# Kernel tuning notes

Hardware: AMD Instinct MI355X
Metric: run time of the kernel (lower is better)

The kernel has to match this reference:

```python
import jax, jax.numpy as jnp
import numpy as np

B, N, D, H = 4, 2048, 1024, 64

def setup_inputs() -> dict:
    key = jax.random.key(0)
    ks = jax.random.split(key, 7)
    s = D ** -0.5  # torch Linear default init scale ~ U(-1/sqrt(fan_in), ...); scale randn similarly
    return {
        "x":  jax.random.normal(ks[0], (B, N, D), dtype=jnp.float32),
        "Wq": jax.random.normal(ks[1], (D, H), dtype=jnp.float32) * s,
        "bq": jax.random.normal(ks[2], (H,), dtype=jnp.float32) * s,
        "Wk": jax.random.normal(ks[3], (D, H), dtype=jnp.float32) * s,
        "bk": jax.random.normal(ks[4], (H,), dtype=jnp.float32) * s,
        "Wv": jax.random.normal(ks[5], (D, H), dtype=jnp.float32) * s,
        "bv": jax.random.normal(ks[6], (H,), dtype=jnp.float32) * s,
    }

def reference(x, Wq, bq, Wk, bk, Wv, bv):
    head_size = Wq.shape[1]
    q = x @ Wq + bq          # [B, N, H]
    k = x @ Wk + bk          # [B, N, H]
    v = x @ Wv + bv          # [B, N, H]
    scores = jnp.einsum("bid,bjd->bij", q, k)        # [B, N, N]
    # faithful to torch: keep upper triangle (col >= row), then mask exact zeros to -inf
    scores = jnp.triu(scores)
    scores = jnp.where(scores == 0, -jnp.inf, scores)
    attn = jax.nn.softmax(scores * (head_size ** -0.5), axis=-1)  # [B, N, N]
    # out = (V^T @ attn)^T  ==  attn^T @ V
    out = jnp.einsum("bji,bjh->bih", attn, v)         # [B, N, H]
    return out
```

## Files before the change

kernel.cpp:

```cpp
#include <hip/hip_runtime.h>
#include <math.h>

constexpr int kN = 2048;
constexpr int kD = 1024;

typedef __attribute__((ext_vector_type(8))) short bf16x8;
typedef __attribute__((ext_vector_type(4))) short bf16x4;
typedef __attribute__((ext_vector_type(4))) float f32x4;

#define MFMA(a, b, c) __builtin_amdgcn_mfma_f32_16x16x32_bf16(a, b, c, 0, 0, 0)

__device__ __forceinline__ short f2bf(float f) {
    unsigned u = __float_as_uint(f);
    u += 0x7fff + ((u >> 16) & 1);
    return (short)(u >> 16);
}

__device__ __forceinline__ void g2l(void* lds, const void* g, int nbytes, int t) {
    int lane = t & 63, w = t >> 6;
    for (int base = w * 1024; base < nbytes; base += 4096) {
        if (base + lane * 16 < nbytes) {
            __builtin_amdgcn_global_load_lds(
                (const __attribute__((address_space(1))) void*)((const char*)g + base + lane * 16),
                (__attribute__((address_space(3))) void*)((char*)lds + base),
                16, 0, 0);
        }
    }
}

__global__ __launch_bounds__(256) void prep_kernel(
        const float* __restrict__ x,
        const float* __restrict__ Wq, const float* __restrict__ Wk,
        const float* __restrict__ Wv, const float* __restrict__ bq,
        const float* __restrict__ bk, const float* __restrict__ bv,
        short* __restrict__ xb, short* __restrict__ Wt, float* __restrict__ bcat)
{
    int tid = blockIdx.x * 256 + threadIdx.x;
    int stride = gridDim.x * 256;
    for (int e = tid; e < 16 * 8192 * 64; e += stride) {
        int kc = e >> 19;
        int rem = e & 524287;
        int row = rem >> 6, c = rem & 63;
        xb[((size_t)(kc * 8192 + row)) * 72 + c] = f2bf(x[(size_t)row * kD + kc * 64 + c]);
    }
    for (int e = tid; e < 16 * 64 * 192; e += stride) {
        int n = e % 192;
        int rc = e / 192;
        int c = rc & 63, kc = rc >> 6;
        int d = kc * 64 + c;
        float wv = (n < 64) ? Wq[d * 64 + n]
                 : (n < 128) ? Wk[d * 64 + (n - 64)]
                 : Wv[d * 64 + (n - 128)];
        Wt[(kc * 192 + n) * 72 + c] = f2bf(wv);
    }
    if (tid < 192)
        bcat[tid] = (tid < 64) ? bq[tid] : (tid < 128) ? bk[tid - 64] : bv[tid - 128];
}

__global__ __launch_bounds__(256) void qkv_kernel(
        const short* __restrict__ xb, const short* __restrict__ Wt,
        const float* __restrict__ bcat,
        short* __restrict__ gq, short* __restrict__ gk, short* __restrict__ vt)
{
    __shared__ __align__(16) short xs[32 * 72];
    __shared__ __align__(16) short wsm[192 * 72];
    const int t = threadIdx.x;
    const int w = t >> 6, lane = t & 63, l15 = lane & 15, q8 = lane >> 4;
    const int m0 = blockIdx.x * 32;

    f32x4 acc[2][3];
    #pragma unroll
    for (int rt = 0; rt < 2; ++rt)
        #pragma unroll
        for (int ct = 0; ct < 3; ++ct) acc[rt][ct] = (f32x4){0.f, 0.f, 0.f, 0.f};

    for (int kc = 0; kc < 16; ++kc) {
        __syncthreads();
        g2l(xs, xb + ((size_t)(kc * 8192 + m0)) * 72, 32 * 144, t);
        g2l(wsm, Wt + (size_t)kc * 192 * 72, 192 * 144, t);
        __syncthreads();

        bf16x8 a[2][2], b[3][2];
        #pragma unroll
        for (int rt = 0; rt < 2; ++rt) {
            int arow = rt * 16 + l15;
            a[rt][0] = *(const bf16x8*)&xs[arow * 72 + q8 * 8];
            a[rt][1] = *(const bf16x8*)&xs[arow * 72 + 32 + q8 * 8];
        }
        #pragma unroll
        for (int ct = 0; ct < 3; ++ct) {
            int brow = w * 48 + ct * 16 + l15;
            b[ct][0] = *(const bf16x8*)&wsm[brow * 72 + q8 * 8];
            b[ct][1] = *(const bf16x8*)&wsm[brow * 72 + 32 + q8 * 8];
        }
        #pragma unroll
        for (int rt = 0; rt < 2; ++rt)
            #pragma unroll
            for (int ct = 0; ct < 3; ++ct) {
                acc[rt][ct] = MFMA(a[rt][0], b[ct][0], acc[rt][ct]);
                acc[rt][ct] = MFMA(a[rt][1], b[ct][1], acc[rt][ct]);
            }
    }

    const int bz = m0 >> 11;
    const int jt = (m0 & 2047) >> 6;
    const int jb = m0 & 63;
    #pragma unroll
    for (int rt = 0; rt < 2; ++rt)
        #pragma unroll
        for (int ct = 0; ct < 3; ++ct) {
            int nb = w * 48 + ct * 16;
            int n = nb + l15;
            float bias = bcat[n];
            if (nb < 64) {
                #pragma unroll
                for (int r = 0; r < 4; ++r)
                    gq[(size_t)(m0 + rt * 16 + q8 * 4 + r) * 72 + n] =
                        f2bf(acc[rt][ct][r] + bias);
            } else if (nb < 128) {
                #pragma unroll
                for (int r = 0; r < 4; ++r)
                    gk[(size_t)(m0 + rt * 16 + q8 * 4 + r) * 72 + (n - 64)] =
                        f2bf(acc[rt][ct][r] + bias);
            } else {
                int h = n - 128;
                bf16x4 pk = {f2bf(acc[rt][ct][0] + bias), f2bf(acc[rt][ct][1] + bias),
                             f2bf(acc[rt][ct][2] + bias), f2bf(acc[rt][ct][3] + bias)};
                *(bf16x4*)&vt[((size_t)((bz * 32 + jt) * 64 + h)) * 72 + jb + rt * 16 + q8 * 4] = pk;
            }
        }
}

__global__ __launch_bounds__(256) void stats_kernel(
        const short* __restrict__ gq, const short* __restrict__ gk,
        float* __restrict__ l2)
{
    __shared__ __align__(16) short qsm[64 * 72];
    __shared__ __align__(16) short ksm[64 * 72];
    const int t = threadIdx.x;
    const int w = t >> 6, lane = t & 63, l15 = lane & 15, q8 = lane >> 4;
    const int b = blockIdx.x;
    const int ic = b & 3, bz = (b >> 2) & 3, jt = b >> 4;
    const int j0 = jt * 64;
    const int ilo = ic * 512, ihi = ilo + 512;
    const int istart = (j0 > ilo) ? j0 : ilo;

    float lloc[4] = {0.f, 0.f, 0.f, 0.f};

    if (istart < ihi) {
        g2l(qsm, gq + (size_t)(bz * kN + j0) * 72, 64 * 144, t);
        __syncthreads();
        int jrow = 16 * w + l15;
        bf16x8 a0 = *(const bf16x8*)&qsm[jrow * 72 + q8 * 8];
        bf16x8 a1 = *(const bf16x8*)&qsm[jrow * 72 + 32 + q8 * 8];

        for (int i0 = istart; i0 < ihi; i0 += 64) {
            __syncthreads();
            g2l(ksm, gk + (size_t)(bz * kN + i0) * 72, 64 * 144, t);
            __syncthreads();
            #pragma unroll
            for (int it = 0; it < 4; ++it) {
                int irow = it * 16 + l15;
                bf16x8 b0 = *(const bf16x8*)&ksm[irow * 72 + q8 * 8];
                bf16x8 b1 = *(const bf16x8*)&ksm[irow * 72 + 32 + q8 * 8];
                f32x4 s = (f32x4){0.f, 0.f, 0.f, 0.f};
                s = MFMA(a0, b0, s);
                s = MFMA(a1, b1, s);
                int ig = i0 + it * 16 + l15;
                #pragma unroll
                for (int r = 0; r < 4; ++r) {
                    int jg = j0 + 16 * w + q8 * 4 + r;
                    float sv = s[r];
                    float e = __expf(sv * 0.125f);
                    lloc[r] += ((ig >= jg) && (sv != 0.0f)) ? e : 0.0f;
                }
            }
        }
    }
    #pragma unroll
    for (int off = 1; off < 16; off <<= 1)
        #pragma unroll
        for (int r = 0; r < 4; ++r)
            lloc[r] += __shfl_xor(lloc[r], off);
    if (l15 == 0) {
        #pragma unroll
        for (int r = 0; r < 4; ++r)
            l2[ic * 8192 + bz * kN + j0 + 16 * w + q8 * 4 + r] = lloc[r];
    }
}

__global__ __launch_bounds__(256) void combine_kernel(
        const float* __restrict__ l2, float* __restrict__ rlf)
{
    int r = blockIdx.x * 256 + threadIdx.x;
    float l = l2[r] + l2[8192 + r] + l2[16384 + r] + l2[24576 + r];
    rlf[r] = (l > 0.f) ? 1.0f / l : 0.0f;
}

__global__ __launch_bounds__(256) void out_kernel(
        const short* __restrict__ gq, const short* __restrict__ gk,
        const short* __restrict__ vt, const float* __restrict__ rlf,
        float* __restrict__ part)
{
    __shared__ __align__(16) short ksm[64 * 72];
    __shared__ __align__(16) short qsm[64 * 72];
    __shared__ __align__(16) short vsm[64 * 72];
    __shared__ __align__(16) short psm[64 * 72];
    __shared__ float rsm[64];
    const int t = threadIdx.x;
    const int w = t >> 6, lane = t & 63, l15 = lane & 15, q8 = lane >> 4;
    const int b = blockIdx.x;
    const int jc = b & 3, bz = (b >> 2) & 3, it = b >> 4;
    const int i0 = it * 64;
    const int jlo = jc * 512;
    const int jhi = (jlo + 512 < i0 + 64) ? (jlo + 512) : (i0 + 64);

    f32x4 oacc[4];
    #pragma unroll
    for (int i = 0; i < 4; ++i) oacc[i] = (f32x4){0.f, 0.f, 0.f, 0.f};

    if (jlo < jhi) {
        g2l(ksm, gk + (size_t)(bz * kN + i0) * 72, 64 * 144, t);
        for (int j0s = jlo; j0s < jhi; j0s += 64) {
            __syncthreads();
            g2l(qsm, gq + (size_t)(bz * kN + j0s) * 72, 64 * 144, t);
            g2l(vsm, vt + (size_t)((bz * 32 + (j0s >> 6)) * 64) * 72, 64 * 144, t);
            if (t < 64) rsm[t] = rlf[bz * kN + j0s + t];
            __syncthreads();

            int jrow = 16 * w + l15;
            bf16x8 a0 = *(const bf16x8*)&qsm[jrow * 72 + q8 * 8];
            bf16x8 a1 = *(const bf16x8*)&qsm[jrow * 72 + 32 + q8 * 8];
            #pragma unroll
            for (int itile = 0; itile < 4; ++itile) {
                int irow = itile * 16 + l15;
                bf16x8 b0 = *(const bf16x8*)&ksm[irow * 72 + q8 * 8];
                bf16x8 b1 = *(const bf16x8*)&ksm[irow * 72 + 32 + q8 * 8];
                f32x4 s = (f32x4){0.f, 0.f, 0.f, 0.f};
                s = MFMA(a0, b0, s);
                s = MFMA(a1, b1, s);
                int ig = i0 + itile * 16 + l15;
                bf16x4 pk;
                #pragma unroll
                for (int r = 0; r < 4; ++r) {
                    int jl = 16 * w + q8 * 4 + r;
                    int jg = j0s + jl;
                    float sv = s[r];
                    float p = ((ig >= jg) && (sv != 0.0f))
                            ? __expf(sv * 0.125f) * rsm[jl] : 0.0f;
                    pk[r] = f2bf(p);
                }
                *(bf16x4*)&psm[(itile * 16 + l15) * 72 + 16 * w + q8 * 4] = pk;
            }
            __syncthreads();

            bf16x8 pa0 = *(const bf16x8*)&psm[(16 * w + l15) * 72 + q8 * 8];
            bf16x8 pa1 = *(const bf16x8*)&psm[(16 * w + l15) * 72 + 32 + q8 * 8];
            #pragma unroll
            for (int ht = 0; ht < 4; ++ht) {
                int vrow = ht * 16 + l15;
                bf16x8 vb0 = *(const bf16x8*)&vsm[vrow * 72 + q8 * 8];
                bf16x8 vb1 = *(const bf16x8*)&vsm[vrow * 72 + 32 + q8 * 8];
                oacc[ht] = MFMA(pa0, vb0, oacc[ht]);
                oacc[ht] = MFMA(pa1, vb1, oacc[ht]);
            }
        }
    }
    size_t base = ((size_t)(jc * 4 + bz) * kN + i0) * 64;
    #pragma unroll
    for (int ht = 0; ht < 4; ++ht)
        #pragma unroll
        for (int r = 0; r < 4; ++r)
            part[base + (size_t)(16 * w + q8 * 4 + r) * 64 + ht * 16 + l15] = oacc[ht][r];
}

__global__ __launch_bounds__(256) void reduce_kernel(
        const float* __restrict__ part, float* __restrict__ out)
{
    int idx = blockIdx.x * 256 + threadIdx.x;
    const float4* p = (const float4*)part;
    float4 a = p[idx];
    float4 b = p[idx + 131072];
    float4 c = p[idx + 262144];
    float4 d = p[idx + 393216];
    float4 r;
    r.x = a.x + b.x + c.x + d.x;
    r.y = a.y + b.y + c.y + d.y;
    r.z = a.z + b.z + c.z + d.z;
    r.w = a.w + b.w + c.w + d.w;
    ((float4*)out)[idx] = r;
}

extern "C" void kernel_launch(void* const* d_in, const int* in_sizes, int n_in,
                              void* d_out, int out_size, void* d_ws, size_t ws_size,
                              hipStream_t stream)
{
    const float* x  = (const float*)d_in[0];
    const float* Wq = (const float*)d_in[1];
    const float* bq = (const float*)d_in[2];
    const float* Wk = (const float*)d_in[3];
    const float* bk = (const float*)d_in[4];
    const float* Wv = (const float*)d_in[5];
    const float* bv = (const float*)d_in[6];
    float* out = (float*)d_out;

    char* base = (char*)d_ws;
    short* Wt   = (short*)(base);
    float* bcat = (float*)(base + 442368);
    short* xb   = (short*)(base + 443392);
    short* gq   = (short*)(base + 19317760);
    short* gk   = (short*)(base + 20497408);
    short* vt   = (short*)(base + 21677056);
    float* l2   = (float*)(base + 22856704);
    float* rlf  = (float*)(base + 22987776);
    float* part = (float*)(base + 23020544);

    prep_kernel<<<2048, 256, 0, stream>>>(x, Wq, Wk, Wv, bq, bk, bv, xb, Wt, bcat);
    qkv_kernel<<<256, 256, 0, stream>>>(xb, Wt, bcat, gq, gk, vt);
    stats_kernel<<<512, 256, 0, stream>>>(gq, gk, l2);
    combine_kernel<<<32, 256, 0, stream>>>(l2, rlf);
    out_kernel<<<512, 256, 0, stream>>>(gq, gk, vt, rlf, part);
    reduce_kernel<<<512, 256, 0, stream>>>(part, out);
}
```

Measured before the change: 143.1 us.

## Fuse x conversion into QKV GEMM, double-buffer LDS loads, drop combine kernel

The separate pass that converted x to a padded bf16 copy is removed. The QKV kernel now loads fp32 x directly, converts it in registers and double-buffers both the x and weight tiles, with 16-row blocks giving twice as many blocks. The stats and out kernels double-buffer their K, Q and V tile loads so the next tile's global loads overlap the current MFMAs. The combine kernel is folded into out_kernel, which computes the reciprocal normalizer inline, saving one launch and a large intermediate write and read of x, at the cost of more LDS per block and redundant reciprocal work.

```diff
diff --git a/kernel.cpp b/kernel.cpp
--- a/kernel.cpp
+++ b/kernel.cpp
@@ -29,106 +29,104 @@
 }
 
 __global__ __launch_bounds__(256) void prep_kernel(
-        const float* __restrict__ x,
         const float* __restrict__ Wq, const float* __restrict__ Wk,
         const float* __restrict__ Wv, const float* __restrict__ bq,
         const float* __restrict__ bk, const float* __restrict__ bv,
-        short* __restrict__ xb, short* __restrict__ Wt, float* __restrict__ bcat)
+        short* __restrict__ Wt, float* __restrict__ bcat)
 {
     int tid = blockIdx.x * 256 + threadIdx.x;
     int stride = gridDim.x * 256;
-    for (int e = tid; e < 16 * 8192 * 64; e += stride) {
-        int kc = e >> 19;
-        int rem = e & 524287;
-        int row = rem >> 6, c = rem & 63;
-        xb[((size_t)(kc * 8192 + row)) * 72 + c] = f2bf(x[(size_t)row * kD + kc * 64 + c]);
-    }
-    for (int e = tid; e < 16 * 64 * 192; e += stride) {
-        int n = e % 192;
-        int rc = e / 192;
-        int c = rc & 63, kc = rc >> 6;
-        int d = kc * 64 + c;
-        float wv = (n < 64) ? Wq[d * 64 + n]
-                 : (n < 128) ? Wk[d * 64 + (n - 64)]
-                 : Wv[d * 64 + (n - 128)];
-        Wt[(kc * 192 + n) * 72 + c] = f2bf(wv);
+    for (int e = tid; e < 16 * 192 * 72; e += stride) {
+        int kc = e / (192 * 72);
+        int rem = e - kc * (192 * 72);
+        int n = rem / 72, c = rem - n * 72;
+        short v = 0;
+        if (c < 64) {
+            int d = kc * 64 + c;
+            float wv = (n < 64) ? Wq[d * 64 + n]
+                     : (n < 128) ? Wk[d * 64 + (n - 64)]
+                     : Wv[d * 64 + (n - 128)];
+            v = f2bf(wv);
+        }
+        Wt[e] = v;
     }
     if (tid < 192)
         bcat[tid] = (tid < 64) ? bq[tid] : (tid < 128) ? bk[tid - 64] : bv[tid - 128];
 }
 
 __global__ __launch_bounds__(256) void qkv_kernel(
-        const short* __restrict__ xb, const short* __restrict__ Wt,
+        const float* __restrict__ x, const short* __restrict__ Wt,
         const float* __restrict__ bcat,
         short* __restrict__ gq, short* __restrict__ gk, short* __restrict__ vt)
 {
-    __shared__ __align__(16) short xs[32 * 72];
-    __shared__ __align__(16) short wsm[192 * 72];
+    __shared__ __align__(16) short xs[2][16 * 72];
+    __shared__ __align__(16) short wsm[2][192 * 72];
     const int t = threadIdx.x;
     const int w = t >> 6, lane = t & 63, l15 = lane & 15, q8 = lane >> 4;
-    const int m0 = blockIdx.x * 32;
-
-    f32x4 acc[2][3];
-    #pragma unroll
-    for (int rt = 0; rt < 2; ++rt)
-        #pragma unroll
-        for (int ct = 0; ct < 3; ++ct) acc[rt][ct] = (f32x4){0.f, 0.f, 0.f, 0.f};
+    const int m0 = blockIdx.x * 16;
+    const int xrow = t >> 4, xc4 = t & 15;
+    const float* xbase = x + (size_t)(m0 + xrow) * kD + xc4 * 4;
+
+    f32x4 acc[3];
+    #pragma unroll
+    for (int ct = 0; ct < 3; ++ct) acc[ct] = (f32x4){0.f, 0.f, 0.f, 0.f};
+
+    float4 xcur = *(const float4*)(xbase + 0 * 64);
+    g2l(wsm[0], Wt, 192 * 144, t);
+    {
+        bf16x4 pk = {f2bf(xcur.x), f2bf(xcur.y), f2bf(xcur.z), f2bf(xcur.w)};
+        *(bf16x4*)&xs[0][xrow * 72 + xc4 * 4] = pk;
+    }
+    float4 xnxt = *(const float4*)(xbase + 1 * 64);
+    __syncthreads();
 
     for (int kc = 0; kc < 16; ++kc) {
-        __syncthreads();
-        g2l(xs, xb + ((size_t)(kc * 8192 + m0)) * 72, 32 * 144, t);
-        g2l(wsm, Wt + (size_t)kc * 192 * 72, 192 * 144, t);
-        __syncthreads();
-
-        bf16x8 a[2][2], b[3][2];
-        #pragma unroll
-        for (int rt = 0; rt < 2; ++rt) {
-            int arow = rt * 16 + l15;
-            a[rt][0] = *(const bf16x8*)&xs[arow * 72 + q8 * 8];
-            a[rt][1] = *(const bf16x8*)&xs[arow * 72 + 32 + q8 * 8];
-        }
+        const int cur = kc & 1, nb = cur ^ 1;
+        if (kc < 15)
+            g2l(wsm[nb], Wt + (size_t)(kc + 1) * 192 * 72, 192 * 144, t);
+
+        bf16x8 a0 = *(const bf16x8*)&xs[cur][l15 * 72 + q8 * 8];
+        bf16x8 a1 = *(const bf16x8*)&xs[cur][l15 * 72 + 32 + q8 * 8];
         #pragma unroll
         for (int ct = 0; ct < 3; ++ct) {
             int brow = w * 48 + ct * 16 + l15;
-            b[ct][0] = *(const bf16x8*)&wsm[brow * 72 + q8 * 8];
-            b[ct][1] = *(const bf16x8*)&wsm[brow * 72 + 32 + q8 * 8];
-        }
-        #pragma unroll
-        for (int rt = 0; rt < 2; ++rt)
-            #pragma unroll
-            for (int ct = 0; ct < 3; ++ct) {
-                acc[rt][ct] = MFMA(a[rt][0], b[ct][0], acc[rt][ct]);
-                acc[rt][ct] = MFMA(a[rt][1], b[ct][1], acc[rt][ct]);
-            }
+            bf16x8 b0 = *(const bf16x8*)&wsm[cur][brow * 72 + q8 * 8];
+            bf16x8 b1 = *(const bf16x8*)&wsm[cur][brow * 72 + 32 + q8 * 8];
+            acc[ct] = MFMA(a0, b0, acc[ct]);
+            acc[ct] = MFMA(a1, b1, acc[ct]);
+        }
+        if (kc < 15) {
+            bf16x4 pk = {f2bf(xnxt.x), f2bf(xnxt.y), f2bf(xnxt.z), f2bf(xnxt.w)};
+            *(bf16x4*)&xs[nb][xrow * 72 + xc4 * 4] = pk;
+            if (kc < 14)
+                xnxt = *(const float4*)(xbase + (kc + 2) * 64);
+        }
+        __syncthreads();
     }
 
     const int bz = m0 >> 11;
     const int jt = (m0 & 2047) >> 6;
     const int jb = m0 & 63;
     #pragma unroll
-    for (int rt = 0; rt < 2; ++rt)
-        #pragma unroll
-        for (int ct = 0; ct < 3; ++ct) {
-            int nb = w * 48 + ct * 16;
-            int n = nb + l15;
-            float bias = bcat[n];
-            if (nb < 64) {
-                #pragma unroll
-                for (int r = 0; r < 4; ++r)
-                    gq[(size_t)(m0 + rt * 16 + q8 * 4 + r) * 72 + n] =
-                        f2bf(acc[rt][ct][r] + bias);
-            } else if (nb < 128) {
-                #pragma unroll
-                for (int r = 0; r < 4; ++r)
-                    gk[(size_t)(m0 + rt * 16 + q8 * 4 + r) * 72 + (n - 64)] =
-                        f2bf(acc[rt][ct][r] + bias);
-            } else {
-                int h = n - 128;
-                bf16x4 pk = {f2bf(acc[rt][ct][0] + bias), f2bf(acc[rt][ct][1] + bias),
-                             f2bf(acc[rt][ct][2] + bias), f2bf(acc[rt][ct][3] + bias)};
-                *(bf16x4*)&vt[((size_t)((bz * 32 + jt) * 64 + h)) * 72 + jb + rt * 16 + q8 * 4] = pk;
-            }
-        }
+    for (int ct = 0; ct < 3; ++ct) {
+        int nb2 = w * 48 + ct * 16;
+        int n = nb2 + l15;
+        float bias = bcat[n];
+        if (nb2 < 64) {
+            #pragma unroll
+            for (int r = 0; r < 4; ++r)
+                gq[(size_t)(m0 + q8 * 4 + r) * 72 + n] = f2bf(acc[ct][r] + bias);
+        } else if (nb2 < 128) {
+            #pragma unroll
+            for (int r = 0; r < 4; ++r)
+                gk[(size_t)(m0 + q8 * 4 + r) * 72 + (n - 64)] = f2bf(acc[ct][r] + bias);
+        } else {
+            int h = n - 128;
+            bf16x4 pk = {f2bf(acc[ct][0] + bias), f2bf(acc[ct][1] + bias),
+                         f2bf(acc[ct][2] + bias), f2bf(acc[ct][3] + bias)};
+            *(bf16x4*)&vt[((size_t)((bz * 32 + jt) * 64 + h)) * 72 + jb + q8 * 4] = pk;
+        }
+    }
 }
 
 __global__ __launch_bounds__(256) void stats_kernel(
@@ -136,7 +134,7 @@
         float* __restrict__ l2)
 {
     __shared__ __align__(16) short qsm[64 * 72];
-    __shared__ __align__(16) short ksm[64 * 72];
+    __shared__ __align__(16) short ksm[2][64 * 72];
     const int t = threadIdx.x;
     const int w = t >> 6, lane = t & 63, l15 = lane & 15, q8 = lane >> 4;
     const int b = blockIdx.x;
@@ -144,25 +142,29 @@
     const int j0 = jt * 64;
     const int ilo = ic * 512, ihi = ilo + 512;
     const int istart = (j0 > ilo) ? j0 : ilo;
+    const int count = (istart < ihi) ? ((ihi - istart) >> 6) : 0;
 
     float lloc[4] = {0.f, 0.f, 0.f, 0.f};
 
-    if (istart < ihi) {
+    if (count > 0) {
         g2l(qsm, gq + (size_t)(bz * kN + j0) * 72, 64 * 144, t);
+        g2l(ksm[0], gk + (size_t)(bz * kN + istart) * 72, 64 * 144, t);
         __syncthreads();
         int jrow = 16 * w + l15;
         bf16x8 a0 = *(const bf16x8*)&qsm[jrow * 72 + q8 * 8];
         bf16x8 a1 = *(const bf16x8*)&qsm[jrow * 72 + 32 + q8 * 8];
 
-        for (int i0 = istart; i0 < ihi; i0 += 64) {
-            __syncthreads();
-            g2l(ksm, gk + (size_t)(bz * kN + i0) * 72, 64 * 144, t);
-            __syncthreads();
+        for (int idx = 0; idx < count; ++idx) {
+            const int cur = idx & 1;
+            if (idx + 1 < count)
+                g2l(ksm[cur ^ 1],
+                    gk + (size_t)(bz * kN + istart + (idx + 1) * 64) * 72, 64 * 144, t);
+            const int i0 = istart + idx * 64;
             #pragma unroll
             for (int it = 0; it < 4; ++it) {
                 int irow = it * 16 + l15;
-                bf16x8 b0 = *(const bf16x8*)&ksm[irow * 72 + q8 * 8];
-                bf16x8 b1 = *(const bf16x8*)&ksm[irow * 72 + 32 + q8 * 8];
+                bf16x8 b0 = *(const bf16x8*)&ksm[cur][irow * 72 + q8 * 8];
+                bf16x8 b1 = *(const bf16x8*)&ksm[cur][irow * 72 + 32 + q8 * 8];
                 f32x4 s = (f32x4){0.f, 0.f, 0.f, 0.f};
                 s = MFMA(a0, b0, s);
                 s = MFMA(a1, b1, s);
@@ -175,6 +177,7 @@
                     lloc[r] += ((ig >= jg) && (sv != 0.0f)) ? e : 0.0f;
                 }
             }
+            __syncthreads();
         }
     }
     #pragma unroll
@@ -189,24 +192,16 @@
     }
 }
 
-__global__ __launch_bounds__(256) void combine_kernel(
-        const float* __restrict__ l2, float* __restrict__ rlf)
-{
-    int r = blockIdx.x * 256 + threadIdx.x;
-    float l = l2[r] + l2[8192 + r] + l2[16384 + r] + l2[24576 + r];
-    rlf[r] = (l > 0.f) ? 1.0f / l : 0.0f;
-}
-
 __global__ __launch_bounds__(256) void out_kernel(
         const short* __restrict__ gq, const short* __restrict__ gk,
-        const short* __restrict__ vt, const float* __restrict__ rlf,
+        const short* __restrict__ vt, const float* __restrict__ l2,
         float* __restrict__ part)
 {
     __shared__ __align__(16) short ksm[64 * 72];
-    __shared__ __align__(16) short qsm[64 * 72];
-    __shared__ __align__(16) short vsm[64 * 72];
+    __shared__ __align__(16) short qsm[2][64 * 72];
+    __shared__ __align__(16) short vsm[2][64 * 72];
     __shared__ __align__(16) short psm[64 * 72];
-    __shared__ float rsm[64];
+    __shared__ float rsm[2][64];
     const int t = threadIdx.x;
     const int w = t >> 6, lane = t & 63, l15 = lane & 15, q8 = lane >> 4;
     const int b = blockIdx.x;
@@ -214,23 +209,39 @@
     const int i0 = it * 64;
     const int jlo = jc * 512;
     const int jhi = (jlo + 512 < i0 + 64) ? (jlo + 512) : (i0 + 64);
+    const int count = (jlo < jhi) ? ((jhi - jlo) >> 6) : 0;
 
     f32x4 oacc[4];
     #pragma unroll
     for (int i = 0; i < 4; ++i) oacc[i] = (f32x4){0.f, 0.f, 0.f, 0.f};
 
-    if (jlo < jhi) {
+    if (count > 0) {
         g2l(ksm, gk + (size_t)(bz * kN + i0) * 72, 64 * 144, t);
-        for (int j0s = jlo; j0s < jhi; j0s += 64) {
-            __syncthreads();
-            g2l(qsm, gq + (size_t)(bz * kN + j0s) * 72, 64 * 144, t);
-            g2l(vsm, vt + (size_t)((bz * 32 + (j0s >> 6)) * 64) * 72, 64 * 144, t);
-            if (t < 64) rsm[t] = rlf[bz * kN + j0s + t];
-            __syncthreads();
-
+        g2l(qsm[0], gq + (size_t)(bz * kN + jlo) * 72, 64 * 144, t);
+        g2l(vsm[0], vt + (size_t)((bz * 32 + (jlo >> 6)) * 64) * 72, 64 * 144, t);
+        if (t < 64) {
+            int j = bz * kN + jlo + t;
+            float l = l2[j] + l2[8192 + j] + l2[16384 + j] + l2[24576 + j];
+            rsm[0][t] = (l > 0.f) ? 1.0f / l : 0.0f;
+        }
+        __syncthreads();
+
+        for (int idx = 0; idx < count; ++idx) {
+            const int cur = idx & 1, nb = cur ^ 1;
+            const int j0s = jlo + idx * 64;
+            if (idx + 1 < count) {
+                g2l(qsm[nb], gq + (size_t)(bz * kN + j0s + 64) * 72, 64 * 144, t);
+                g2l(vsm[nb], vt + (size_t)((bz * 32 + ((j0s + 64) >> 6)) * 64) * 72,
+                    64 * 144, t);
+                if (t < 64) {
+                    int j = bz * kN + j0s + 64 + t;
+                    float l = l2[j] + l2[8192 + j] + l2[16384 + j] + l2[24576 + j];
+                    rsm[nb][t] = (l > 0.f) ? 1.0f / l : 0.0f;
+                }
+            }
             int jrow = 16 * w + l15;
-            bf16x8 a0 = *(const bf16x8*)&qsm[jrow * 72 + q8 * 8];
-            bf16x8 a1 = *(const bf16x8*)&qsm[jrow * 72 + 32 + q8 * 8];
+            bf16x8 a0 = *(const bf16x8*)&qsm[cur][jrow * 72 + q8 * 8];
+            bf16x8 a1 = *(const bf16x8*)&qsm[cur][jrow * 72 + 32 + q8 * 8];
             #pragma unroll
             for (int itile = 0; itile < 4; ++itile) {
                 int irow = itile * 16 + l15;
@@ -247,7 +258,7 @@
                     int jg = j0s + jl;
                     float sv = s[r];
                     float p = ((ig >= jg) && (sv != 0.0f))
-                            ? __expf(sv * 0.125f) * rsm[jl] : 0.0f;
+                            ? __expf(sv * 0.125f) * rsm[cur][jl] : 0.0f;
                     pk[r] = f2bf(p);
                 }
                 *(bf16x4*)&psm[(itile * 16 + l15) * 72 + 16 * w + q8 * 4] = pk;
@@ -259,11 +270,12 @@
             #pragma unroll
             for (int ht = 0; ht < 4; ++ht) {
                 int vrow = ht * 16 + l15;
-                bf16x8 vb0 = *(const bf16x8*)&vsm[vrow * 72 + q8 * 8];
-                bf16x8 vb1 = *(const bf16x8*)&vsm[vrow * 72 + 32 + q8 * 8];
+                bf16x8 vb0 = *(const bf16x8*)&vsm[cur][vrow * 72 + q8 * 8];
+                bf16x8 vb1 = *(const bf16x8*)&vsm[cur][vrow * 72 + 32 + q8 * 8];
                 oacc[ht] = MFMA(pa0, vb0, oacc[ht]);
                 oacc[ht] = MFMA(pa1, vb1, oacc[ht]);
             }
+            __syncthreads();
         }
     }
     size_t base = ((size_t)(jc * 4 + bz) * kN + i0) * 64;
@@ -307,18 +319,15 @@
     char* base = (char*)d_ws;
     short* Wt   = (short*)(base);
     float* bcat = (float*)(base + 442368);
-    short* xb   = (short*)(base + 443392);
-    short* gq   = (short*)(base + 19317760);
-    short* gk   = (short*)(base + 20497408);
-    short* vt   = (short*)(base + 21677056);
-    float* l2   = (float*)(base + 22856704);
-    float* rlf  = (float*)(base + 22987776);
-    float* part = (float*)(base + 23020544);
-
-    prep_kernel<<<2048, 256, 0, stream>>>(x, Wq, Wk, Wv, bq, bk, bv, xb, Wt, bcat);
-    qkv_kernel<<<256, 256, 0, stream>>>(xb, Wt, bcat, gq, gk, vt);
+    short* gq   = (short*)(base + 443392);
+    short* gk   = (short*)(base + 1623040);
+    short* vt   = (short*)(base + 2802688);
+    float* l2   = (float*)(base + 3982336);
+    float* part = (float*)(base + 4113408);
+
+    prep_kernel<<<128, 256, 0, stream>>>(Wq, Wk, Wv, bq, bk, bv, Wt, bcat);
+    qkv_kernel<<<512, 256, 0, stream>>>(x, Wt, bcat, gq, gk, vt);
     stats_kernel<<<512, 256, 0, stream>>>(gq, gk, l2);
-    combine_kernel<<<32, 256, 0, stream>>>(l2, rlf);
-    out_kernel<<<512, 256, 0, stream>>>(gq, gk, vt, rlf, part);
+    out_kernel<<<512, 256, 0, stream>>>(gq, gk, vt, l2, part);
     reduce_kernel<<<512, 256, 0, stream>>>(part, out);
 }
```

After: 134.9 us. 5.8% less time.
